# Kernel optimization log

Measured on AMD Instinct MI355X. Metric: run time of the kernel, lower is better.

## Reference

```python
import jax, jax.numpy as jnp
import numpy as np

VOCAB = 32000
D_VEC = 1024

def setup_inputs() -> dict:
    key = jax.random.key(0)
    kq, ke = jax.random.split(key)
    q = jax.random.normal(kq, (4, 1024, D_VEC), dtype=jnp.float32)
    # emb_matrix ~ Uniform(-0.1, 0.1), as in torch .uniform_(-0.1, 0.1)
    emb_matrix = jax.random.uniform(ke, (VOCAB, D_VEC), dtype=jnp.float32,
                                    minval=-0.1, maxval=0.1)
    return {"q": q, "emb_matrix": emb_matrix}

def reference(q, emb_matrix):
    # scores: [B, L, V] = q @ emb^T  (unscaled single-head attention)
    scores = jnp.einsum('bld,vd->blv', q, emb_matrix)
    attn = jax.nn.softmax(scores, axis=-1)
    # dropout is identity in eval / deterministic reference
    ctx = jnp.einsum('blv,vd->bld', attn, emb_matrix)
    return ctx + q
```

## Files before the change

### kernel.cpp

```cpp
#include <hip/hip_runtime.h>
#include <hip/hip_bf16.h>

#define D_DIM 1024
#define VOCABSZ 32000
#define NROWSZ 4096
#define MBLK 64
#define LOG2E 1.44269504088896340736f

typedef unsigned short u16;
typedef short s8v __attribute__((ext_vector_type(8)));
typedef short s4v __attribute__((ext_vector_type(4)));
typedef float f4v __attribute__((ext_vector_type(4)));
typedef __attribute__((address_space(3))) const char* lds_p3;

static __device__ __forceinline__ u16 f2bf(float f) {
  union { float f; unsigned int u; } x; x.f = f;
  unsigned int r = x.u + 0x7fffu + ((x.u >> 16) & 1u);
  return (u16)(r >> 16);
}
static __device__ __forceinline__ unsigned int pack2(float lo, float hi) {
  return (unsigned int)f2bf(lo) | ((unsigned int)f2bf(hi) << 16);
}
static __device__ __forceinline__ unsigned int pk_rn(float lo, float hi) {
  float2 f; f.x = lo; f.y = hi;
  union { __hip_bfloat162 h; unsigned int u; } v;
  v.h = __float22bfloat162_rn(f);
  return v.u;
}
#define EXP2(x) __builtin_amdgcn_exp2f(x)

static __device__ __forceinline__ float bf2f(u16 b) {
  union { unsigned int u; float f; } x; x.u = ((unsigned int)b) << 16;
  return x.f;
}
static __device__ __forceinline__ float bfu_lo(unsigned int u) {
  union { unsigned int u; float f; } x; x.u = u << 16; return x.f;
}
static __device__ __forceinline__ float bfu_hi(unsigned int u) {
  union { unsigned int u; float f; } x; x.u = u & 0xffff0000u; return x.f;
}
static __device__ __forceinline__ f4v MFMA(s8v a, s8v b, f4v c) {
  return __builtin_amdgcn_mfma_f32_16x16x32_bf16(a, b, c, 0, 0, 0);
}

#define GLOAD_LDS16(gp, lp)                                                  \
  __builtin_amdgcn_global_load_lds(                                         \
      (const __attribute__((address_space(1))) void*)(gp),                  \
      (__attribute__((address_space(3))) void*)(lp), 16, 0, 0)

__global__ __launch_bounds__(256) void cvt3_kernel(const float* __restrict__ emb,
                                                   char* __restrict__ ETt) {
  const int b = blockIdx.x, t = threadIdx.x;
  const int v0 = b * 32;
  char* outp = ETt + ((size_t)b << 16);
#pragma unroll
  for (int k = 0; k < 16; ++k) {
    int ci = t + 256 * k;
    int v = ci >> 7;
    int d8 = ci & 127;
    const float* s = emb + (size_t)(v0 + v) * D_DIM + d8 * 8;
    float4 a = *(const float4*)s;
    float4 bb = *(const float4*)(s + 4);
    uint4 x;
    x.x = pack2(a.x, a.y); x.y = pack2(a.z, a.w);
    x.z = pack2(bb.x, bb.y); x.w = pack2(bb.z, bb.w);
    int off = ((v >> 2) * 64 + (d8 >> 1)) * 128 + (v & 3) * 32 + (d8 & 1) * 16;
    *(uint4*)(outp + off) = x;
  }
}

template <int NSPLIT>
__global__ __launch_bounds__(512, 2) void flash12_kernel(
    const float* __restrict__ qg, const char* __restrict__ ETt,
    float* __restrict__ out, u16* __restrict__ pctx, float* __restrict__ pstat) {
  __shared__ char ring[2 * 65536];
  __shared__ uint2 Sred[8 * 4 * 64];
  __shared__ char Plds[4096];
  __shared__ float lred[8][16];

  const int tid = threadIdx.x;
  const int w = tid >> 6;
  const int l = tid & 63;
  const int g = l >> 4;
  const int c = l & 15;
  const int ds = w & 3;
  const int mh = w >> 2;
  const int bid = blockIdx.x;
  const int sp = (NSPLIT == 4) ? (bid & 3) : 0;
  const int rb = (NSPLIT == 4) ? (bid >> 2) : bid;
  const int row0 = rb * MBLK;
  const int vslice = VOCABSZ / NSPLIT;
  const int ntiles = vslice / 32;
  const int gt0 = sp * ntiles;

  const f4v fzero = {0.f, 0.f, 0.f, 0.f};

  s8v qf[2][8];
#pragma unroll
  for (int mt = 0; mt < 2; ++mt)
#pragma unroll
    for (int kt = 0; kt < 8; ++kt) {
      const float* src = qg + (size_t)(row0 + mh * 32 + 16 * mt + c) * D_DIM +
                         ds * 256 + 32 * kt + 8 * g;
      float4 a = *(const float4*)src;
      float4 b = *(const float4*)(src + 4);
      s8v v;
      v[0] = (short)f2bf(a.x * LOG2E); v[1] = (short)f2bf(a.y * LOG2E);
      v[2] = (short)f2bf(a.z * LOG2E); v[3] = (short)f2bf(a.w * LOG2E);
      v[4] = (short)f2bf(b.x * LOG2E); v[5] = (short)f2bf(b.y * LOG2E);
      v[6] = (short)f2bf(b.z * LOG2E); v[7] = (short)f2bf(b.w * LOG2E);
      qf[mt][kt] = v;
    }

  f4v acc[2][16];
#pragma unroll
  for (int mt = 0; mt < 2; ++mt)
#pragma unroll
    for (int nt = 0; nt < 16; ++nt) acc[mt][nt] = fzero;

  float lcur = 0.f;

#define STAGE(U)                                                             \
  {                                                                          \
    const char* _gs = ETt + (((size_t)(gt0 + (U))) << 16) + tid * 16;        \
    char* _ls = ring + (((U) & 1) << 16) + tid * 16;                         \
    _Pragma("unroll") for (int _j = 0; _j < 8; ++_j)                         \
        GLOAD_LDS16(_gs + _j * 8192, _ls + _j * 8192);                       \
  }

  STAGE(0);
  __syncthreads();

  for (int t = 0; t < ntiles; ++t) {
    const char* buf = ring + ((t & 1) << 16);

#pragma unroll
    for (int vt = 0; vt < 2; ++vt) {
      const char* bp = buf + (((4 * vt + (c >> 2)) * 64 + 16 * ds + (g >> 1)) * 128 +
                              (c & 3) * 32 + (g & 1) * 16);
      f4v st0a = fzero, st0b = fzero, st1a = fzero, st1b = fzero;
#pragma unroll
      for (int kt = 0; kt < 4; ++kt) {
        s8v ek = *(const s8v*)(bp + kt * 256);
        st0a = MFMA(ek, qf[0][kt], st0a);
        st1a = MFMA(ek, qf[1][kt], st1a);
      }
#pragma unroll
      for (int kt = 4; kt < 8; ++kt) {
        s8v ek = *(const s8v*)(bp + kt * 256);
        st0b = MFMA(ek, qf[0][kt], st0b);
        st1b = MFMA(ek, qf[1][kt], st1b);
      }
      f4v st0 = st0a + st0b;
      f4v st1 = st1a + st1b;
      int qb = ((mh * 4 + vt * 2) * 4 + ds) * 64 + l;
      uint2 pk;
      pk.x = pk_rn(st0[0], st0[1]); pk.y = pk_rn(st0[2], st0[3]);
      Sred[qb] = pk;
      pk.x = pk_rn(st1[0], st1[1]); pk.y = pk_rn(st1[2], st1[3]);
      Sred[qb + 256] = pk;
    }
    __syncthreads();

    {
      int qq = mh * 4 + ds;
      f4v ss = fzero;
#pragma unroll
      for (int ww = 0; ww < 4; ++ww) {
        uint2 u = Sred[(qq * 4 + ww) * 64 + l];
        ss[0] += bfu_lo(u.x); ss[1] += bfu_hi(u.x);
        ss[2] += bfu_lo(u.y); ss[3] += bfu_hi(u.y);
      }
      float p0 = EXP2(ss[0]), p1 = EXP2(ss[1]);
      float p2 = EXP2(ss[2]), p3 = EXP2(ss[3]);
      int pb = mh * 2048 + (16 * (ds & 1) + c) * 64 + (16 * (ds >> 1) + 4 * g) * 2;
      uint2 pw; pw.x = pk_rn(p0, p1); pw.y = pk_rn(p2, p3);
      *(uint2*)(Plds + pb) = pw;
      lcur += (p0 + p1) + (p2 + p3);
    }
    __syncthreads();

    if (t + 1 < ntiles) STAGE(t + 1);

    {
      int pab = mh * 2048 + c * 64 + g * 16;
      s8v pa0 = *(const s8v*)(Plds + pab);
      s8v pa1 = *(const s8v*)(Plds + pab + 1024);
#pragma unroll
      for (int bb = 0; bb < 2; ++bb) {
        union { s4v s[2]; s8v v; } ev[8];
#pragma unroll
        for (int k = 0; k < 8; ++k) {
          int nt = bb * 8 + k;
          const char* a0 = buf + ((2 * g) * 64 + 16 * ds + nt) * 128 + c * 2;
          asm volatile("ds_read_b64_tr_b16 %0, %1"
                       : "=v"(ev[k].s[0]) : "v"((lds_p3)a0));
          asm volatile("ds_read_b64_tr_b16 %0, %1"
                       : "=v"(ev[k].s[1]) : "v"((lds_p3)(a0 + 8192)));
        }
        asm volatile("s_waitcnt lgkmcnt(0)" ::: "memory");
        __builtin_amdgcn_sched_barrier(0);
#pragma unroll
        for (int k = 0; k < 8; ++k) {
          int nt = bb * 8 + k;
          acc[0][nt] = MFMA(pa0, ev[k].v, acc[0][nt]);
          acc[1][nt] = MFMA(pa1, ev[k].v, acc[1][nt]);
        }
      }
    }
  }
#undef STAGE

  {
    float lp = lcur;
    lp += __shfl_xor(lp, 16);
    lp += __shfl_xor(lp, 32);
    __syncthreads();
    if (g == 0) lred[mh * 4 + ds][c] = lp;
  }
  __syncthreads();

  if (NSPLIT == 1) {
#pragma unroll
    for (int mt = 0; mt < 2; ++mt) {
      float inv[4];
#pragma unroll
      for (int r = 0; r < 4; ++r)
        inv[r] = 1.f / (lred[mh * 4 + mt][4 * g + r] + lred[mh * 4 + 2 + mt][4 * g + r]);
#pragma unroll
      for (int nt = 0; nt < 16; ++nt)
#pragma unroll
        for (int r = 0; r < 4; ++r) {
          size_t o = (size_t)(row0 + mh * 32 + 16 * mt + 4 * g + r) * D_DIM +
                     ds * 256 + 16 * nt + c;
          out[o] = acc[mt][nt][r] * inv[r] + qg[o];
        }
    }
  } else {
    u16* pc = pctx + (size_t)sp * NROWSZ * D_DIM;
#pragma unroll
    for (int mt = 0; mt < 2; ++mt)
#pragma unroll
      for (int nt = 0; nt < 16; ++nt)
#pragma unroll
        for (int r = 0; r < 4; ++r)
          pc[(size_t)(row0 + mh * 32 + 16 * mt + 4 * g + r) * D_DIM +
             ds * 256 + 16 * nt + c] = f2bf(acc[mt][nt][r]);
    if (ds < 2 && g == 0)
      pstat[(size_t)sp * NROWSZ + row0 + mh * 32 + 16 * ds + c] =
          lred[mh * 4 + ds][c] + lred[mh * 4 + 2 + ds][c];
  }
}

__global__ __launch_bounds__(256) void combine2_kernel(const float* __restrict__ qg,
                                                       const u16* __restrict__ pctx,
                                                       const float* __restrict__ pstat,
                                                       float* __restrict__ out) {
  const int r = blockIdx.x;
  const int t = threadIdx.x;
  float L = pstat[r] + pstat[NROWSZ + r] + pstat[2 * NROWSZ + r] + pstat[3 * NROWSZ + r];
  float inv = 1.f / L;
  size_t o = (size_t)r * D_DIM + t * 4;
  float sx = 0.f, sy = 0.f, sz = 0.f, sw = 0.f;
#pragma unroll
  for (int sp = 0; sp < 4; ++sp) {
    ushort4 u = *(const ushort4*)(pctx + (size_t)sp * NROWSZ * D_DIM + o);
    sx += bf2f(u.x); sy += bf2f(u.y); sz += bf2f(u.z); sw += bf2f(u.w);
  }
  float4 qv = *(const float4*)(qg + o);
  float4 res;
  res.x = sx * inv + qv.x;
  res.y = sy * inv + qv.y;
  res.z = sz * inv + qv.z;
  res.w = sw * inv + qv.w;
  *(float4*)(out + o) = res;
}

__global__ __launch_bounds__(256) void naive_kernel(const float* __restrict__ qg,
                                                    const float* __restrict__ emb,
                                                    float* __restrict__ out) {
  __shared__ float s[VOCABSZ];
  __shared__ float qrow[D_DIM];
  __shared__ float lsh[4];
  const int r = blockIdx.x;
  const int t = threadIdx.x;
  for (int i = t; i < D_DIM; i += 256) qrow[i] = qg[(size_t)r * D_DIM + i];
  __syncthreads();
  float lpart = 0.f;
  for (int v = t; v < VOCABSZ; v += 256) {
    float dot = 0.f;
    for (int d = 0; d < D_DIM; d += 4) {
      float4 e = *(const float4*)(emb + (size_t)v * D_DIM + d);
      dot += qrow[d] * e.x + qrow[d + 1] * e.y + qrow[d + 2] * e.z + qrow[d + 3] * e.w;
    }
    float p = exp2f(dot * LOG2E);
    s[v] = p;
    lpart += p;
  }
  for (int o = 32; o; o >>= 1) lpart += __shfl_xor(lpart, o);
  if ((t & 63) == 0) lsh[t >> 6] = lpart;
  __syncthreads();
  float inv = 1.f / (lsh[0] + lsh[1] + lsh[2] + lsh[3]);
  float ax = 0.f, ay = 0.f, az = 0.f, aw = 0.f;
  for (int v = 0; v < VOCABSZ; ++v) {
    float p = s[v];
    float4 e = *(const float4*)(emb + (size_t)v * D_DIM + t * 4);
    ax += p * e.x; ay += p * e.y; az += p * e.z; aw += p * e.w;
  }
  size_t o = (size_t)r * D_DIM + t * 4;
  float4 qv = *(const float4*)(qg + o);
  float4 res;
  res.x = ax * inv + qv.x;
  res.y = ay * inv + qv.y;
  res.z = az * inv + qv.z;
  res.w = aw * inv + qv.w;
  *(float4*)(out + o) = res;
}

extern "C" void kernel_launch(void* const* d_in, const int* in_sizes, int n_in,
                              void* d_out, int out_size, void* d_ws, size_t ws_size,
                              hipStream_t stream) {
  const float* q = (const float*)d_in[0];
  const float* emb = (const float*)d_in[1];
  float* out = (float*)d_out;
  char* ws = (char*)d_ws;

  const size_t ETT_BYTES = 65536000ull;
  const size_t PCTX_BYTES = 4ull * NROWSZ * D_DIM * 2;
  const size_t PSTAT_BYTES = 4ull * NROWSZ * 4;

  if (ws_size >= ETT_BYTES + PCTX_BYTES + PSTAT_BYTES) {
    char* ETt = ws;
    u16* pctx = (u16*)(ws + ETT_BYTES);
    float* pstat = (float*)(ws + ETT_BYTES + PCTX_BYTES);
    cvt3_kernel<<<VOCABSZ / 32, 256, 0, stream>>>(emb, ETt);
    flash12_kernel<4><<<256, 512, 0, stream>>>(q, ETt, out, pctx, pstat);
    combine2_kernel<<<NROWSZ, 256, 0, stream>>>(q, pctx, pstat, out);
  } else if (ws_size >= ETT_BYTES) {
    char* ETt = ws;
    cvt3_kernel<<<VOCABSZ / 32, 256, 0, stream>>>(emb, ETt);
    flash12_kernel<1><<<NROWSZ / MBLK, 512, 0, stream>>>(q, ETt, out, nullptr, nullptr);
  } else {
    naive_kernel<<<NROWSZ, 256, 0, stream>>>(q, emb, out);
  }
}
```

Measured before the change: 607.2 us.

## Repartition waves to split D eight ways across all 64 rows per wave

Each of the 8 waves now owns a 128-wide slice of D for all 64 query rows, instead of a 256-wide slice for 32 rows. Every emb fragment read from LDS is therefore reused across 4 row tiles in both the score and the context MFMAs, which halves LDS read traffic per MFMA. The cost is a cross-wave score reduction that grows from 4 to 8 partials, with 7 bf16 partials going through a larger Sred buffer. The P buffer in LDS is also XOR-swizzled to avoid bank conflicts.

```diff
diff --git a/kernel.cpp b/kernel.cpp
--- a/kernel.cpp
+++ b/kernel.cpp
@@ -70,21 +70,18 @@
 }
 
 template <int NSPLIT>
-__global__ __launch_bounds__(512, 2) void flash12_kernel(
+__global__ __launch_bounds__(512, 2) void flash15_kernel(
     const float* __restrict__ qg, const char* __restrict__ ETt,
     float* __restrict__ out, u16* __restrict__ pctx, float* __restrict__ pstat) {
   __shared__ char ring[2 * 65536];
-  __shared__ uint2 Sred[8 * 4 * 64];
+  __shared__ uint2 Sred[8 * 7 * 64];
   __shared__ char Plds[4096];
-  __shared__ float lred[8][16];
 
   const int tid = threadIdx.x;
   const int w = tid >> 6;
   const int l = tid & 63;
   const int g = l >> 4;
   const int c = l & 15;
-  const int ds = w & 3;
-  const int mh = w >> 2;
   const int bid = blockIdx.x;
   const int sp = (NSPLIT == 4) ? (bid & 3) : 0;
   const int rb = (NSPLIT == 4) ? (bid >> 2) : bid;
@@ -94,14 +91,15 @@
   const int gt0 = sp * ntiles;
 
   const f4v fzero = {0.f, 0.f, 0.f, 0.f};
-
-  s8v qf[2][8];
-#pragma unroll
-  for (int mt = 0; mt < 2; ++mt)
-#pragma unroll
-    for (int kt = 0; kt < 8; ++kt) {
-      const float* src = qg + (size_t)(row0 + mh * 32 + 16 * mt + c) * D_DIM +
-                         ds * 256 + 32 * kt + 8 * g;
+  const int swzP = (((c & 3) ^ ((c >> 2) & 1)) << 4);
+
+  s8v qf[4][4];
+#pragma unroll
+  for (int mt = 0; mt < 4; ++mt)
+#pragma unroll
+    for (int kt = 0; kt < 4; ++kt) {
+      const float* src = qg + (size_t)(row0 + 16 * mt + c) * D_DIM +
+                         w * 128 + 32 * kt + 8 * g;
       float4 a = *(const float4*)src;
       float4 b = *(const float4*)(src + 4);
       s8v v;
@@ -112,12 +110,13 @@
       qf[mt][kt] = v;
     }
 
-  f4v acc[2][16];
-#pragma unroll
-  for (int mt = 0; mt < 2; ++mt)
-#pragma unroll
-    for (int nt = 0; nt < 16; ++nt) acc[mt][nt] = fzero;
-
+  f4v acc[4][8];
+#pragma unroll
+  for (int mt = 0; mt < 4; ++mt)
+#pragma unroll
+    for (int nt = 0; nt < 8; ++nt) acc[mt][nt] = fzero;
+
+  f4v ssown = fzero;
   float lcur = 0.f;
 
 #define STAGE(U)                                                             \
@@ -136,44 +135,46 @@
 
 #pragma unroll
     for (int vt = 0; vt < 2; ++vt) {
-      const char* bp = buf + (((4 * vt + (c >> 2)) * 64 + 16 * ds + (g >> 1)) * 128 +
+      const char* bp = buf + (((4 * vt + (c >> 2)) * 64 + 8 * w + (g >> 1)) * 128 +
                               (c & 3) * 32 + (g & 1) * 16);
-      f4v st0a = fzero, st0b = fzero, st1a = fzero, st1b = fzero;
+      f4v st[4];
+      st[0] = fzero; st[1] = fzero; st[2] = fzero; st[3] = fzero;
 #pragma unroll
       for (int kt = 0; kt < 4; ++kt) {
         s8v ek = *(const s8v*)(bp + kt * 256);
-        st0a = MFMA(ek, qf[0][kt], st0a);
-        st1a = MFMA(ek, qf[1][kt], st1a);
+        st[0] = MFMA(ek, qf[0][kt], st[0]);
+        st[1] = MFMA(ek, qf[1][kt], st[1]);
+        st[2] = MFMA(ek, qf[2][kt], st[2]);
+        st[3] = MFMA(ek, qf[3][kt], st[3]);
       }
 #pragma unroll
-      for (int kt = 4; kt < 8; ++kt) {
-        s8v ek = *(const s8v*)(bp + kt * 256);
-        st0b = MFMA(ek, qf[0][kt], st0b);
-        st1b = MFMA(ek, qf[1][kt], st1b);
+      for (int mt = 0; mt < 4; ++mt) {
+        const int q = vt * 4 + mt;
+        if (q == w) {
+          ssown = st[mt];
+        } else {
+          int slot = w - (w > q ? 1 : 0);
+          uint2 pk;
+          pk.x = pk_rn(st[mt][0], st[mt][1]);
+          pk.y = pk_rn(st[mt][2], st[mt][3]);
+          Sred[(q * 7 + slot) * 64 + l] = pk;
+        }
       }
-      f4v st0 = st0a + st0b;
-      f4v st1 = st1a + st1b;
-      int qb = ((mh * 4 + vt * 2) * 4 + ds) * 64 + l;
-      uint2 pk;
-      pk.x = pk_rn(st0[0], st0[1]); pk.y = pk_rn(st0[2], st0[3]);
-      Sred[qb] = pk;
-      pk.x = pk_rn(st1[0], st1[1]); pk.y = pk_rn(st1[2], st1[3]);
-      Sred[qb + 256] = pk;
     }
     __syncthreads();
 
     {
-      int qq = mh * 4 + ds;
-      f4v ss = fzero;
-#pragma unroll
-      for (int ww = 0; ww < 4; ++ww) {
-        uint2 u = Sred[(qq * 4 + ww) * 64 + l];
+      f4v ss = ssown;
+#pragma unroll
+      for (int s = 0; s < 7; ++s) {
+        uint2 u = Sred[(w * 7 + s) * 64 + l];
         ss[0] += bfu_lo(u.x); ss[1] += bfu_hi(u.x);
         ss[2] += bfu_lo(u.y); ss[3] += bfu_hi(u.y);
       }
       float p0 = EXP2(ss[0]), p1 = EXP2(ss[1]);
       float p2 = EXP2(ss[2]), p3 = EXP2(ss[3]);
-      int pb = mh * 2048 + (16 * (ds & 1) + c) * 64 + (16 * (ds >> 1) + 4 * g) * 2;
+      int m_ = 16 * (w & 3) + c;
+      int pb = m_ * 64 + ((32 * (w >> 2) + 8 * g) ^ swzP);
       uint2 pw; pw.x = pk_rn(p0, p1); pw.y = pk_rn(p2, p3);
       *(uint2*)(Plds + pb) = pw;
       lcur += (p0 + p1) + (p2 + p3);
@@ -183,16 +184,18 @@
     if (t + 1 < ntiles) STAGE(t + 1);
 
     {
-      int pab = mh * 2048 + c * 64 + g * 16;
-      s8v pa0 = *(const s8v*)(Plds + pab);
-      s8v pa1 = *(const s8v*)(Plds + pab + 1024);
+      const int prb = c * 64 + ((16 * g) ^ swzP);
+      s8v pa0 = *(const s8v*)(Plds + prb);
+      s8v pa1 = *(const s8v*)(Plds + prb + 1024);
+      s8v pa2 = *(const s8v*)(Plds + prb + 2048);
+      s8v pa3 = *(const s8v*)(Plds + prb + 3072);
+      const char* ab = buf + g * 16384 + w * 1024 + c * 2;
 #pragma unroll
       for (int bb = 0; bb < 2; ++bb) {
-        union { s4v s[2]; s8v v; } ev[8];
-#pragma unroll
-        for (int k = 0; k < 8; ++k) {
-          int nt = bb * 8 + k;
-          const char* a0 = buf + ((2 * g) * 64 + 16 * ds + nt) * 128 + c * 2;
+        union uev { s4v s[2]; s8v v; } ev[4];
+#pragma unroll
+        for (int k = 0; k < 4; ++k) {
+          const char* a0 = ab + (bb * 4 + k) * 128;
           asm volatile("ds_read_b64_tr_b16 %0, %1"
                        : "=v"(ev[k].s[0]) : "v"((lds_p3)a0));
           asm volatile("ds_read_b64_tr_b16 %0, %1"
@@ -201,54 +204,57 @@
         asm volatile("s_waitcnt lgkmcnt(0)" ::: "memory");
         __builtin_amdgcn_sched_barrier(0);
 #pragma unroll
-        for (int k = 0; k < 8; ++k) {
-          int nt = bb * 8 + k;
+        for (int k = 0; k < 4; ++k) {
+          int nt = bb * 4 + k;
           acc[0][nt] = MFMA(pa0, ev[k].v, acc[0][nt]);
           acc[1][nt] = MFMA(pa1, ev[k].v, acc[1][nt]);
+          acc[2][nt] = MFMA(pa2, ev[k].v, acc[2][nt]);
+          acc[3][nt] = MFMA(pa3, ev[k].v, acc[3][nt]);
         }
       }
     }
   }
 #undef STAGE
 
+  float* lredp = (float*)Sred;
   {
     float lp = lcur;
     lp += __shfl_xor(lp, 16);
     lp += __shfl_xor(lp, 32);
     __syncthreads();
-    if (g == 0) lred[mh * 4 + ds][c] = lp;
+    if (g == 0) lredp[w * 16 + c] = lp;
   }
   __syncthreads();
 
   if (NSPLIT == 1) {
 #pragma unroll
-    for (int mt = 0; mt < 2; ++mt) {
+    for (int mt = 0; mt < 4; ++mt) {
       float inv[4];
 #pragma unroll
       for (int r = 0; r < 4; ++r)
-        inv[r] = 1.f / (lred[mh * 4 + mt][4 * g + r] + lred[mh * 4 + 2 + mt][4 * g + r]);
-#pragma unroll
-      for (int nt = 0; nt < 16; ++nt)
+        inv[r] = 1.f / (lredp[mt * 16 + 4 * g + r] + lredp[(mt + 4) * 16 + 4 * g + r]);
+#pragma unroll
+      for (int nt = 0; nt < 8; ++nt)
 #pragma unroll
         for (int r = 0; r < 4; ++r) {
-          size_t o = (size_t)(row0 + mh * 32 + 16 * mt + 4 * g + r) * D_DIM +
-                     ds * 256 + 16 * nt + c;
+          size_t o = (size_t)(row0 + 16 * mt + 4 * g + r) * D_DIM +
+                     w * 128 + 16 * nt + c;
           out[o] = acc[mt][nt][r] * inv[r] + qg[o];
         }
     }
   } else {
     u16* pc = pctx + (size_t)sp * NROWSZ * D_DIM;
 #pragma unroll
-    for (int mt = 0; mt < 2; ++mt)
-#pragma unroll
-      for (int nt = 0; nt < 16; ++nt)
+    for (int mt = 0; mt < 4; ++mt)
+#pragma unroll
+      for (int nt = 0; nt < 8; ++nt)
 #pragma unroll
         for (int r = 0; r < 4; ++r)
-          pc[(size_t)(row0 + mh * 32 + 16 * mt + 4 * g + r) * D_DIM +
-             ds * 256 + 16 * nt + c] = f2bf(acc[mt][nt][r]);
-    if (ds < 2 && g == 0)
-      pstat[(size_t)sp * NROWSZ + row0 + mh * 32 + 16 * ds + c] =
-          lred[mh * 4 + ds][c] + lred[mh * 4 + 2 + ds][c];
+          pc[(size_t)(row0 + 16 * mt + 4 * g + r) * D_DIM +
+             w * 128 + 16 * nt + c] = f2bf(acc[mt][nt][r]);
+    if (w < 4 && g == 0)
+      pstat[(size_t)sp * NROWSZ + row0 + 16 * w + c] =
+          lredp[w * 16 + c] + lredp[(w + 4) * 16 + c];
   }
 }
 
@@ -334,12 +340,12 @@
     u16* pctx = (u16*)(ws + ETT_BYTES);
     float* pstat = (float*)(ws + ETT_BYTES + PCTX_BYTES);
     cvt3_kernel<<<VOCABSZ / 32, 256, 0, stream>>>(emb, ETt);
-    flash12_kernel<4><<<256, 512, 0, stream>>>(q, ETt, out, pctx, pstat);
+    flash15_kernel<4><<<256, 512, 0, stream>>>(q, ETt, out, pctx, pstat);
     combine2_kernel<<<NROWSZ, 256, 0, stream>>>(q, pctx, pstat, out);
   } else if (ws_size >= ETT_BYTES) {
     char* ETt = ws;
     cvt3_kernel<<<VOCABSZ / 32, 256, 0, stream>>>(emb, ETt);
-    flash12_kernel<1><<<NROWSZ / MBLK, 512, 0, stream>>>(q, ETt, out, nullptr, nullptr);
+    flash15_kernel<1><<<NROWSZ / MBLK, 512, 0, stream>>>(q, ETt, out, nullptr, nullptr);
   } else {
     naive_kernel<<<NROWSZ, 256, 0, stream>>>(q, emb, out);
   }
```

New measurement: 592.9 us. 2.3% less time.
